# Kernel tuning notes

Hardware: AMD Instinct MI355X
Metric: run time of the kernel (lower is better)

The kernel has to match this reference:

```python
import jax, jax.numpy as jnp
import numpy as np

OUT_FEATURES = 64  # self.out_features after list unwrapping


def setup_inputs() -> dict:
    key = jax.random.key(0)
    k1, k2, k3 = jax.random.split(key, 3)
    B, T, N, F = 1, 2, 196608, 32   # zoom 7 -> 12*4^7 HEALPix cells
    K = 9                            # HEALPix neighborhood size (cell + 8 neighbors)
    UP = 4                           # out_zoom - in_zoom = 1 -> 4 child cells
    x = jax.random.normal(k1, (B, T, N, F), dtype=jnp.float32)
    adjc = jax.random.randint(k2, (N, K), 0, N, dtype=jnp.int64)
    W = jax.random.normal(k3, (K, F, UP, OUT_FEATURES), dtype=jnp.float32) / np.sqrt(K * F)
    b = jnp.zeros((UP, OUT_FEATURES), dtype=jnp.float32)
    return {"x": x, "adjc": adjc, "W": W, "b": b}


def reference(x, adjc, W, b):
    # grid_layer.get_nh: gather neighbor features via adjacency -> [B,T,N,K,F]
    nh = x[:, :, adjc, :]
    # learned transform contracting neighborhood (K) and features (F)
    # into 4 child cells (u) x out_features (o)
    out = jnp.einsum('btnkf,kfuo->btnuo', nh, W) + b
    # x.reshape(*x.shape[:3], -1, self.out_features)
    return out.reshape(*out.shape[:3], -1, OUT_FEATURES)
```

## Files before the change

### kernel.cpp

```cpp
#include <hip/hip_runtime.h>

typedef short bf16x8 __attribute__((ext_vector_type(8)));
typedef float f32x4 __attribute__((ext_vector_type(4)));
typedef unsigned short u16;

#define NNODE 196608
#define FF 32
#define COLS 256
#define KTOT 288
#define WELEMS (COLS * KTOT)
#define TPB 6

__device__ __forceinline__ u16 f2bf(float f) {
    unsigned u = __builtin_bit_cast(unsigned, f);
    return (u16)((u + 0x7fffu + ((u >> 16) & 1u)) >> 16);
}

__global__ void cvt_x(const float* __restrict__ x, u16* __restrict__ xb2, int n8) {
    int i = blockIdx.x * blockDim.x + threadIdx.x;
    if (i >= n8) return;
    int og   = i * 8;
    int node = og >> 6;
    int rem  = og & 63;
    int s    = rem >> 5;
    int f0   = rem & 31;
    const float* src = x + ((size_t)s * NNODE + node) * FF + f0;
    f32x4 v0 = *(const f32x4*)src;
    f32x4 v1 = *(const f32x4*)(src + 4);
    union { u16 h[8]; bf16x8 v; } r;
    #pragma unroll
    for (int j = 0; j < 4; ++j) r.h[j] = f2bf(v0[j]);
    #pragma unroll
    for (int j = 0; j < 4; ++j) r.h[4 + j] = f2bf(v1[j]);
    *((bf16x8*)xb2 + i) = r.v;
}

__global__ void cvt_w(const float* __restrict__ W, u16* __restrict__ Wt) {
    int gid = blockIdx.x * 256 + threadIdx.x;
    int f      = gid >> 9;
    int within = gid & 511;
    int lane   = within >> 3;
    int e      = within & 7;
    int kk = f >> 4, ct = f & 15;
    int cl = lane & 15, q = lane >> 4;
    int c  = ct * 16 + cl;
    int kf = kk * 32 + q * 8 + e;
    Wt[gid] = f2bf(W[(size_t)kf * COLS + c]);
}

__global__ __launch_bounds__(512, 2) void updown_main(
    const u16* __restrict__ xb2, const u16* __restrict__ Wt,
    const int* __restrict__ adjc, const float* __restrict__ bias,
    float* __restrict__ out)
{
    __shared__ __align__(16) u16 wlds[WELEMS];
    __shared__ __align__(16) float blds[COLS];

    const int tid = threadIdx.x;

    #pragma unroll
    for (int i = 0; i < 18; ++i)
        *(bf16x8*)(wlds + i * 4096 + tid * 8) =
            *(const bf16x8*)(Wt + i * 4096 + tid * 8);
    if (tid < 64) ((f32x4*)blds)[tid] = ((const f32x4*)bias)[tid];
    __syncthreads();

    const int w    = tid >> 6;
    const int lane = tid & 63;
    const int l15  = lane & 15;
    const int q    = lane >> 4;
    const u16* wbase = wlds + lane * 8;
    const float* bb  = blds + q * 4;

    const int node0 = blockIdx.x * (TPB * 128) + w * 16 + l15;

    for (int tt = 0; tt < TPB; ++tt) {
        const int node  = node0 + tt * 128;
        const int* arow = adjc + (size_t)node * 9;

        int i0 = arow[0];
        int i1 = arow[1];
        const u16* g0 = xb2 + (size_t)i0 * 64 + q * 8;
        bf16x8 aC0 = *(const bf16x8*)g0;
        bf16x8 aC1 = *(const bf16x8*)(g0 + 32);
        const u16* g1 = xb2 + (size_t)i1 * 64 + q * 8;
        bf16x8 aN0 = *(const bf16x8*)g1;
        bf16x8 aN1 = *(const bf16x8*)(g1 + 32);
        int idxP = arow[2];

        f32x4 acc0[16], acc1[16];
        #pragma unroll
        for (int ct = 0; ct < 16; ++ct) {
            f32x4 bq = *(const f32x4*)(bb + ct * 16);
            acc0[ct] = bq;
            acc1[ct] = bq;
        }

        #pragma unroll
        for (int kk = 0; kk < 9; ++kk) {
            bf16x8 aNN0, aNN1;
            if (kk < 7) {
                const u16* g2 = xb2 + (size_t)idxP * 64 + q * 8;
                aNN0 = *(const bf16x8*)g2;
                aNN1 = *(const bf16x8*)(g2 + 32);
            }
            if (kk < 6) idxP = arow[kk + 3];

            const u16* wk = wbase + kk * 8192;
            #pragma unroll
            for (int ct = 0; ct < 16; ++ct) {
                bf16x8 af = *(const bf16x8*)(wk + ct * 512);
                acc0[ct] = __builtin_amdgcn_mfma_f32_16x16x32_bf16(af, aC0, acc0[ct], 0, 0, 0);
                acc1[ct] = __builtin_amdgcn_mfma_f32_16x16x32_bf16(af, aC1, acc1[ct], 0, 0, 0);
            }
            if (kk < 8) { aC0 = aN0; aC1 = aN1; }
            if (kk < 7) { aN0 = aNN0; aN1 = aNN1; }
        }

        float* o0 = out + (size_t)node * COLS + q * 4;
        float* o1 = o0 + (size_t)NNODE * COLS;
        #pragma unroll
        for (int ct = 0; ct < 16; ++ct) {
            *(f32x4*)(o0 + ct * 16) = acc0[ct];
            *(f32x4*)(o1 + ct * 16) = acc1[ct];
        }

        __builtin_amdgcn_s_barrier();
    }
}

extern "C" void kernel_launch(void* const* d_in, const int* in_sizes, int n_in,
                              void* d_out, int out_size, void* d_ws, size_t ws_size,
                              hipStream_t stream) {
    const float* x    = (const float*)d_in[0];
    const int*   adjc = (const int*)d_in[1];
    const float* W    = (const float*)d_in[2];
    const float* b    = (const float*)d_in[3];
    float* out = (float*)d_out;

    u16* xb2 = (u16*)d_ws;
    u16* Wt  = xb2 + (size_t)NNODE * 64;

    cvt_x<<<dim3(6144), dim3(256), 0, stream>>>(x, xb2, 1572864);
    cvt_w<<<dim3(288), dim3(256), 0, stream>>>(W, Wt);
    updown_main<<<dim3(256), dim3(512), 0, stream>>>(xb2, Wt, adjc, b, out);
}
```

Measured before the change: 143.9 us.

## Split time steps across wave pairs and double block size to 1024 threads

Measured after the change: 148.7 us. 1.03x slower.

```diff
diff --git a/kernel.cpp b/kernel.cpp
--- a/kernel.cpp
+++ b/kernel.cpp
@@ -48,7 +48,7 @@
     Wt[gid] = f2bf(W[(size_t)kf * COLS + c]);
 }
 
-__global__ __launch_bounds__(512, 2) void updown_main(
+__global__ __launch_bounds__(1024, 4) void updown_main(
     const u16* __restrict__ xb2, const u16* __restrict__ Wt,
     const int* __restrict__ adjc, const float* __restrict__ bias,
     float* __restrict__ out)
@@ -59,9 +59,9 @@
     const int tid = threadIdx.x;
 
     #pragma unroll
-    for (int i = 0; i < 18; ++i)
-        *(bf16x8*)(wlds + i * 4096 + tid * 8) =
-            *(const bf16x8*)(Wt + i * 4096 + tid * 8);
+    for (int i = 0; i < 9; ++i)
+        *(bf16x8*)(wlds + i * 8192 + tid * 8) =
+            *(const bf16x8*)(Wt + i * 8192 + tid * 8);
     if (tid < 64) ((f32x4*)blds)[tid] = ((const f32x4*)bias)[tid];
     __syncthreads();
 
@@ -69,10 +69,13 @@
     const int lane = tid & 63;
     const int l15  = lane & 15;
     const int q    = lane >> 4;
+    const int g    = w >> 1;
+    const int s    = w & 1;
     const u16* wbase = wlds + lane * 8;
     const float* bb  = blds + q * 4;
+    const u16* xbs   = xb2 + s * 32;
 
-    const int node0 = blockIdx.x * (TPB * 128) + w * 16 + l15;
+    const int node0 = blockIdx.x * (TPB * 128) + g * 16 + l15;
 
     for (int tt = 0; tt < TPB; ++tt) {
         const int node  = node0 + tt * 128;
@@ -80,50 +83,36 @@
 
         int i0 = arow[0];
         int i1 = arow[1];
-        const u16* g0 = xb2 + (size_t)i0 * 64 + q * 8;
-        bf16x8 aC0 = *(const bf16x8*)g0;
-        bf16x8 aC1 = *(const bf16x8*)(g0 + 32);
-        const u16* g1 = xb2 + (size_t)i1 * 64 + q * 8;
-        bf16x8 aN0 = *(const bf16x8*)g1;
-        bf16x8 aN1 = *(const bf16x8*)(g1 + 32);
+        bf16x8 aC = *(const bf16x8*)(xbs + (size_t)i0 * 64 + q * 8);
+        bf16x8 aN = *(const bf16x8*)(xbs + (size_t)i1 * 64 + q * 8);
         int idxP = arow[2];
 
-        f32x4 acc0[16], acc1[16];
+        f32x4 acc[16];
         #pragma unroll
-        for (int ct = 0; ct < 16; ++ct) {
-            f32x4 bq = *(const f32x4*)(bb + ct * 16);
-            acc0[ct] = bq;
-            acc1[ct] = bq;
-        }
+        for (int ct = 0; ct < 16; ++ct)
+            acc[ct] = *(const f32x4*)(bb + ct * 16);
 
         #pragma unroll
         for (int kk = 0; kk < 9; ++kk) {
-            bf16x8 aNN0, aNN1;
-            if (kk < 7) {
-                const u16* g2 = xb2 + (size_t)idxP * 64 + q * 8;
-                aNN0 = *(const bf16x8*)g2;
-                aNN1 = *(const bf16x8*)(g2 + 32);
-            }
+            bf16x8 aNN;
+            if (kk < 7)
+                aNN = *(const bf16x8*)(xbs + (size_t)idxP * 64 + q * 8);
             if (kk < 6) idxP = arow[kk + 3];
 
             const u16* wk = wbase + kk * 8192;
             #pragma unroll
             for (int ct = 0; ct < 16; ++ct) {
                 bf16x8 af = *(const bf16x8*)(wk + ct * 512);
-                acc0[ct] = __builtin_amdgcn_mfma_f32_16x16x32_bf16(af, aC0, acc0[ct], 0, 0, 0);
-                acc1[ct] = __builtin_amdgcn_mfma_f32_16x16x32_bf16(af, aC1, acc1[ct], 0, 0, 0);
+                acc[ct] = __builtin_amdgcn_mfma_f32_16x16x32_bf16(af, aC, acc[ct], 0, 0, 0);
             }
-            if (kk < 8) { aC0 = aN0; aC1 = aN1; }
-            if (kk < 7) { aN0 = aNN0; aN1 = aNN1; }
+            if (kk < 8) aC = aN;
+            if (kk < 7) aN = aNN;
         }
 
-        float* o0 = out + (size_t)node * COLS + q * 4;
-        float* o1 = o0 + (size_t)NNODE * COLS;
+        float* o = out + ((size_t)s * NNODE + node) * COLS + q * 4;
         #pragma unroll
-        for (int ct = 0; ct < 16; ++ct) {
-            *(f32x4*)(o0 + ct * 16) = acc0[ct];
-            *(f32x4*)(o1 + ct * 16) = acc1[ct];
-        }
+        for (int ct = 0; ct < 16; ++ct)
+            *(f32x4*)(o + ct * 16) = acc[ct];
 
         __builtin_amdgcn_s_barrier();
     }
@@ -143,5 +132,5 @@
 
     cvt_x<<<dim3(6144), dim3(256), 0, stream>>>(x, xb2, 1572864);
     cvt_w<<<dim3(288), dim3(256), 0, stream>>>(W, Wt);
-    updown_main<<<dim3(256), dim3(512), 0, stream>>>(xb2, Wt, adjc, b, out);
+    updown_main<<<dim3(256), dim3(1024), 0, stream>>>(xb2, Wt, adjc, b, out);
 }
```

## Prefetch next tile's full neighborhood gather during output stores

Applied to the files above, without the earlier changes.

New measurement: 158.9 us. 1.1x slower.

```diff
diff --git a/kernel.cpp b/kernel.cpp
--- a/kernel.cpp
+++ b/kernel.cpp
@@ -74,19 +74,22 @@
 
     const int node0 = blockIdx.x * (TPB * 128) + w * 16 + l15;
 
+    bf16x8 g0[9], g1[9];
+    {
+        const int* arow = adjc + (size_t)node0 * 9;
+        int idxA[9];
+        #pragma unroll
+        for (int k = 0; k < 9; ++k) idxA[k] = arow[k];
+        #pragma unroll
+        for (int k = 0; k < 9; ++k) {
+            const u16* p = xb2 + (size_t)idxA[k] * 64 + q * 8;
+            g0[k] = *(const bf16x8*)p;
+            g1[k] = *(const bf16x8*)(p + 32);
+        }
+    }
+
     for (int tt = 0; tt < TPB; ++tt) {
-        const int node  = node0 + tt * 128;
-        const int* arow = adjc + (size_t)node * 9;
-
-        int i0 = arow[0];
-        int i1 = arow[1];
-        const u16* g0 = xb2 + (size_t)i0 * 64 + q * 8;
-        bf16x8 aC0 = *(const bf16x8*)g0;
-        bf16x8 aC1 = *(const bf16x8*)(g0 + 32);
-        const u16* g1 = xb2 + (size_t)i1 * 64 + q * 8;
-        bf16x8 aN0 = *(const bf16x8*)g1;
-        bf16x8 aN1 = *(const bf16x8*)(g1 + 32);
-        int idxP = arow[2];
+        const int node = node0 + tt * 128;
 
         f32x4 acc0[16], acc1[16];
         #pragma unroll
@@ -96,26 +99,33 @@
             acc1[ct] = bq;
         }
 
+        int idxN[9];
+        if (tt < TPB - 1) {
+            const int* arow2 = adjc + (size_t)(node + 128) * 9;
+            #pragma unroll
+            for (int k = 0; k < 9; ++k) idxN[k] = arow2[k];
+        }
+
         #pragma unroll
         for (int kk = 0; kk < 9; ++kk) {
-            bf16x8 aNN0, aNN1;
-            if (kk < 7) {
-                const u16* g2 = xb2 + (size_t)idxP * 64 + q * 8;
-                aNN0 = *(const bf16x8*)g2;
-                aNN1 = *(const bf16x8*)(g2 + 32);
-            }
-            if (kk < 6) idxP = arow[kk + 3];
-
             const u16* wk = wbase + kk * 8192;
             #pragma unroll
             for (int ct = 0; ct < 16; ++ct) {
                 bf16x8 af = *(const bf16x8*)(wk + ct * 512);
-                acc0[ct] = __builtin_amdgcn_mfma_f32_16x16x32_bf16(af, aC0, acc0[ct], 0, 0, 0);
-                acc1[ct] = __builtin_amdgcn_mfma_f32_16x16x32_bf16(af, aC1, acc1[ct], 0, 0, 0);
+                acc0[ct] = __builtin_amdgcn_mfma_f32_16x16x32_bf16(af, g0[kk], acc0[ct], 0, 0, 0);
+                acc1[ct] = __builtin_amdgcn_mfma_f32_16x16x32_bf16(af, g1[kk], acc1[ct], 0, 0, 0);
             }
-            if (kk < 8) { aC0 = aN0; aC1 = aN1; }
-            if (kk < 7) { aN0 = aNN0; aN1 = aNN1; }
         }
+
+        if (tt < TPB - 1) {
+            #pragma unroll
+            for (int k = 0; k < 9; ++k) {
+                const u16* p = xb2 + (size_t)idxN[k] * 64 + q * 8;
+                g0[k] = *(const bf16x8*)p;
+                g1[k] = *(const bf16x8*)(p + 32);
+            }
+        }
+        __builtin_amdgcn_sched_barrier(0);
 
         float* o0 = out + (size_t)node * COLS + q * 4;
         float* o1 = o0 + (size_t)NNODE * COLS;
@@ -124,8 +134,6 @@
             *(f32x4*)(o0 + ct * 16) = acc0[ct];
             *(f32x4*)(o1 + ct * 16) = acc1[ct];
         }
-
-        __builtin_amdgcn_s_barrier();
     }
 }
 
```

## Split output columns across wave pairs, each wave handling two node groups

Applied to the files above, without the earlier changes.

After: 156.8 us. +8.9%, slower.

```diff
diff --git a/kernel.cpp b/kernel.cpp
--- a/kernel.cpp
+++ b/kernel.cpp
@@ -69,60 +69,81 @@
     const int lane = tid & 63;
     const int l15  = lane & 15;
     const int q    = lane >> 4;
-    const u16* wbase = wlds + lane * 8;
-    const float* bb  = blds + q * 4;
+    const int ng   = w >> 1;
+    const int ch   = w & 1;
+    const u16* wbase = wlds + (size_t)(ch * 8) * 512 + lane * 8;
+    const float* bb  = blds + ch * 128 + q * 4;
 
-    const int node0 = blockIdx.x * (TPB * 128) + w * 16 + l15;
+    const int node0 = blockIdx.x * (TPB * 128) + ng * 32 + l15;
 
     for (int tt = 0; tt < TPB; ++tt) {
         const int node  = node0 + tt * 128;
-        const int* arow = adjc + (size_t)node * 9;
+        const int* ar0 = adjc + (size_t)node * 9;
+        const int* ar1 = adjc + (size_t)(node + 16) * 9;
 
-        int i0 = arow[0];
-        int i1 = arow[1];
-        const u16* g0 = xb2 + (size_t)i0 * 64 + q * 8;
-        bf16x8 aC0 = *(const bf16x8*)g0;
-        bf16x8 aC1 = *(const bf16x8*)(g0 + 32);
-        const u16* g1 = xb2 + (size_t)i1 * 64 + q * 8;
-        bf16x8 aN0 = *(const bf16x8*)g1;
-        bf16x8 aN1 = *(const bf16x8*)(g1 + 32);
-        int idxP = arow[2];
+        int i00 = ar0[0], i10 = ar1[0];
+        int i01 = ar0[1], i11 = ar1[1];
+        const u16* p00 = xb2 + (size_t)i00 * 64 + q * 8;
+        const u16* p10 = xb2 + (size_t)i10 * 64 + q * 8;
+        const u16* p01 = xb2 + (size_t)i01 * 64 + q * 8;
+        const u16* p11 = xb2 + (size_t)i11 * 64 + q * 8;
+        bf16x8 aC0t0 = *(const bf16x8*)p00, aC0t1 = *(const bf16x8*)(p00 + 32);
+        bf16x8 aC1t0 = *(const bf16x8*)p10, aC1t1 = *(const bf16x8*)(p10 + 32);
+        bf16x8 aN0t0 = *(const bf16x8*)p01, aN0t1 = *(const bf16x8*)(p01 + 32);
+        bf16x8 aN1t0 = *(const bf16x8*)p11, aN1t1 = *(const bf16x8*)(p11 + 32);
+        int idxP0 = ar0[2], idxP1 = ar1[2];
 
-        f32x4 acc0[16], acc1[16];
+        f32x4 a0t0[8], a0t1[8], a1t0[8], a1t1[8];
         #pragma unroll
-        for (int ct = 0; ct < 16; ++ct) {
+        for (int ct = 0; ct < 8; ++ct) {
             f32x4 bq = *(const f32x4*)(bb + ct * 16);
-            acc0[ct] = bq;
-            acc1[ct] = bq;
+            a0t0[ct] = bq; a0t1[ct] = bq;
+            a1t0[ct] = bq; a1t1[ct] = bq;
         }
 
         #pragma unroll
         for (int kk = 0; kk < 9; ++kk) {
-            bf16x8 aNN0, aNN1;
+            bf16x8 aNN0t0, aNN0t1, aNN1t0, aNN1t1;
             if (kk < 7) {
-                const u16* g2 = xb2 + (size_t)idxP * 64 + q * 8;
-                aNN0 = *(const bf16x8*)g2;
-                aNN1 = *(const bf16x8*)(g2 + 32);
+                const u16* g0 = xb2 + (size_t)idxP0 * 64 + q * 8;
+                const u16* g1 = xb2 + (size_t)idxP1 * 64 + q * 8;
+                aNN0t0 = *(const bf16x8*)g0; aNN0t1 = *(const bf16x8*)(g0 + 32);
+                aNN1t0 = *(const bf16x8*)g1; aNN1t1 = *(const bf16x8*)(g1 + 32);
             }
-            if (kk < 6) idxP = arow[kk + 3];
+            if (kk < 6) { idxP0 = ar0[kk + 3]; idxP1 = ar1[kk + 3]; }
 
             const u16* wk = wbase + kk * 8192;
             #pragma unroll
-            for (int ct = 0; ct < 16; ++ct) {
+            for (int ct = 0; ct < 8; ++ct) {
                 bf16x8 af = *(const bf16x8*)(wk + ct * 512);
-                acc0[ct] = __builtin_amdgcn_mfma_f32_16x16x32_bf16(af, aC0, acc0[ct], 0, 0, 0);
-                acc1[ct] = __builtin_amdgcn_mfma_f32_16x16x32_bf16(af, aC1, acc1[ct], 0, 0, 0);
+                a0t0[ct] = __builtin_amdgcn_mfma_f32_16x16x32_bf16(af, aC0t0, a0t0[ct], 0, 0, 0);
+                a0t1[ct] = __builtin_amdgcn_mfma_f32_16x16x32_bf16(af, aC0t1, a0t1[ct], 0, 0, 0);
+                a1t0[ct] = __builtin_amdgcn_mfma_f32_16x16x32_bf16(af, aC1t0, a1t0[ct], 0, 0, 0);
+                a1t1[ct] = __builtin_amdgcn_mfma_f32_16x16x32_bf16(af, aC1t1, a1t1[ct], 0, 0, 0);
             }
-            if (kk < 8) { aC0 = aN0; aC1 = aN1; }
-            if (kk < 7) { aN0 = aNN0; aN1 = aNN1; }
+            if (kk < 8) {
+                aC0t0 = aN0t0; aC0t1 = aN0t1;
+                aC1t0 = aN1t0; aC1t1 = aN1t1;
+            }
+            if (kk < 7) {
+                aN0t0 = aNN0t0; aN0t1 = aNN0t1;
+                aN1t0 = aNN1t0; aN1t1 = aNN1t1;
+            }
         }
 
-        float* o0 = out + (size_t)node * COLS + q * 4;
-        float* o1 = o0 + (size_t)NNODE * COLS;
-        #pragma unroll
-        for (int ct = 0; ct < 16; ++ct) {
-            *(f32x4*)(o0 + ct * 16) = acc0[ct];
-            *(f32x4*)(o1 + ct * 16) = acc1[ct];
+        {
+            float* o = out + (size_t)node * COLS + ch * 128 + q * 4;
+            float* p0 = o;
+            float* p1 = o + (size_t)NNODE * COLS;
+            float* p2 = o + 16 * COLS;
+            float* p3 = p2 + (size_t)NNODE * COLS;
+            #pragma unroll
+            for (int ct = 0; ct < 8; ++ct) {
+                *(f32x4*)(p0 + ct * 16) = a0t0[ct];
+                *(f32x4*)(p1 + ct * 16) = a0t1[ct];
+                *(f32x4*)(p2 + ct * 16) = a1t0[ct];
+                *(f32x4*)(p3 + ct * 16) = a1t1[ct];
+            }
         }
 
         __builtin_amdgcn_s_barrier();
```
